# Performance work log

Hardware: AMD Instinct MI355X
Metric: run time of the kernel (lower is better)

## Reference

```python
import jax, jax.numpy as jnp
import numpy as np

N = 2_000_000
NODES = 16
FEAT = 19  # 9 (F) + 9 (cof F) + 1 (det F)


def setup_inputs() -> dict:
    key = jax.random.key(0)
    ks = jax.random.split(key, 9)
    # well-conditioned deformation gradients: F = I + 0.1*randn
    Fs = jnp.eye(3, dtype=jnp.float32) + 0.1 * jax.random.normal(ks[0], (N, 3, 3), dtype=jnp.float32)
    def glorot(k, shape):
        fan_in, fan_out = shape
        lim = np.sqrt(6.0 / (fan_in + fan_out)).astype(np.float32)
        return jax.random.uniform(k, shape, jnp.float32, -lim, lim)
    # layer 0: Dense(16, softplus); layers 1,2: Dense(16, softplus, non_neg kernel);
    # layer 3: Dense(1, linear, non_neg kernel). non_neg is a constraint applied
    # during training; we emulate by taking abs of the constrained kernels.
    W1 = glorot(ks[1], (FEAT, NODES)); b1 = jnp.zeros((NODES,), jnp.float32)
    W2 = jnp.abs(glorot(ks[2], (NODES, NODES))); b2 = jnp.zeros((NODES,), jnp.float32)
    W3 = jnp.abs(glorot(ks[3], (NODES, NODES))); b3 = jnp.zeros((NODES,), jnp.float32)
    W4 = jnp.abs(glorot(ks[4], (NODES, 1))); b4 = jnp.zeros((1,), jnp.float32)
    return {"Fs": Fs, "W1": W1, "b1": b1, "W2": W2, "b2": b2,
            "W3": W3, "b3": b3, "W4": W4, "b4": b4}


def _features(Fs):
    # det via closed-form 3x3 expansion (same value as tf.linalg.det)
    a, b, c = Fs[:, 0, 0], Fs[:, 0, 1], Fs[:, 0, 2]
    d, e, f = Fs[:, 1, 0], Fs[:, 1, 1], Fs[:, 1, 2]
    g, h, i = Fs[:, 2, 0], Fs[:, 2, 1], Fs[:, 2, 2]
    det = a * (e * i - f * h) - b * (d * i - f * g) + c * (d * h - e * g)
    # cof(F) = inv(F)^T * det  (original: transpose(inv(F)) @ diag(tile(det,3)))
    cof = jnp.swapaxes(jnp.linalg.inv(Fs), 1, 2) * det[:, None, None]
    # [N,19] = flat(F) ++ flat(cof) ++ det
    return jnp.concatenate([Fs.reshape(-1, 9), cof.reshape(-1, 9), det[:, None]], axis=1)


def reference(Fs, W1, b1, W2, b2, W3, b3, W4, b4):
    x = _features(Fs)
    x = jax.nn.softplus(x @ W1 + b1)
    x = jax.nn.softplus(x @ W2 + b2)
    x = jax.nn.softplus(x @ W3 + b3)
    return x @ W4 + b4  # [N,1]
```

## Files before the change

kernel.cpp:

```cpp
#include <hip/hip_runtime.h>
#include <hip/hip_fp16.h>
#include <math.h>

#define TPB 256
#define NODES 16
#define BLOCKS 2048

typedef float f32x4 __attribute__((ext_vector_type(4)));
typedef _Float16 half4 __attribute__((ext_vector_type(4)));
typedef _Float16 h2 __attribute__((ext_vector_type(2)));

#define LOG2E 1.44269504088896340736f
#define LN2   0.69314718055994530942f

__device__ __forceinline__ _Float16 hx2(_Float16 x) {
    __half h = __builtin_bit_cast(__half, x);
    __half r = hexp2(h);
    return __builtin_bit_cast(_Float16, r);
}

__device__ __forceinline__ unsigned int sp2_pos(float v0, float v1) {
    h2 h = __builtin_bit_cast(h2, __builtin_amdgcn_cvt_pkrtz(v0, v1));
    h2 e = { hx2((_Float16)(-h[0])), hx2((_Float16)(-h[1])) };
    const h2 c3 = {(_Float16)0.154358f,  (_Float16)0.154358f};
    const h2 c2 = {(_Float16)-0.571177f, (_Float16)-0.571177f};
    const h2 c1 = {(_Float16)1.416467f,  (_Float16)1.416467f};
    const h2 c0 = {(_Float16)0.000837f,  (_Float16)0.000837f};
    h2 p = __builtin_elementwise_fma(e,
             __builtin_elementwise_fma(e,
               __builtin_elementwise_fma(e, c3, c2), c1), c0);
    h2 r = h + p;
    return __builtin_bit_cast(unsigned int, r);
}
__device__ __forceinline__ unsigned int sp2_any(float v0, float v1) {
    h2 h = __builtin_bit_cast(h2, __builtin_amdgcn_cvt_pkrtz(v0, v1));
    const h2 z = {(_Float16)0.0f, (_Float16)0.0f};
    h2 m  = __builtin_elementwise_max(h, z);
    h2 nt = __builtin_elementwise_min(h, z - h);
    h2 e = { hx2(nt[0]), hx2(nt[1]) };
    const h2 c3 = {(_Float16)0.154358f,  (_Float16)0.154358f};
    const h2 c2 = {(_Float16)-0.571177f, (_Float16)-0.571177f};
    const h2 c1 = {(_Float16)1.416467f,  (_Float16)1.416467f};
    const h2 c0 = {(_Float16)0.000837f,  (_Float16)0.000837f};
    h2 p = __builtin_elementwise_fma(e,
             __builtin_elementwise_fma(e,
               __builtin_elementwise_fma(e, c3, c2), c1), c0);
    h2 r = m + p;
    return __builtin_bit_cast(unsigned int, r);
}
__device__ __forceinline__ unsigned int pk2(float a, float b) {
    return __builtin_bit_cast(unsigned int, __builtin_amdgcn_cvt_pkrtz(a, b));
}
__device__ __forceinline__ half4 h4(uint2 u) {
    return __builtin_bit_cast(half4, u);
}

__global__ __launch_bounds__(TPB, 4) void mlp_mfma_kernel(
    const float* __restrict__ Fs,
    const float* __restrict__ W1, const float* __restrict__ b1,
    const float* __restrict__ W2, const float* __restrict__ b2,
    const float* __restrict__ W3, const float* __restrict__ b3,
    const float* __restrict__ W4, const float* __restrict__ b4,
    float* __restrict__ out, int n, int iters)
{
    __shared__ uint2 lds[4][320];
    const int tid = threadIdx.x;
    const int l = tid & 63, w = tid >> 6;
    const int g = l >> 4, c = l & 15;

    half4 a1lo, a1hi, a2, a3, a4;
    f32x4 cb1, cb2, cb3, cb4;
    #pragma unroll
    for (int j = 0; j < 4; ++j) {
        a1lo[j] = (_Float16)(W1[(4*g+j)*NODES + c] * LOG2E);
        a1hi[j] = (_Float16)((g == 0 && j < 3) ? W1[(16+j)*NODES + c] * LOG2E : 0.0f);
        a2[j]   = (_Float16)W2[(4*g+j)*NODES + c];
        a3[j]   = (_Float16)W3[(4*g+j)*NODES + c];
        a4[j]   = (_Float16)(W4[4*g+j] * LN2);
    }
    const float b4s = b4[0];
    #pragma unroll
    for (int i = 0; i < 4; ++i) {
        cb1[i] = b1[4*g+i] * LOG2E;
        cb2[i] = b2[4*g+i] * LOG2E;
        cb3[i] = b3[4*g+i] * LOG2E;
        cb4[i] = b4s;
    }

    uint2* basep = &lds[w][0];
    const long long s0 = ((long long)blockIdx.x * 4 + w) * (64LL * iters);
    if (s0 >= n) return;

    float fr[9];
    {
        long long sE = s0 + l; if (sE > n - 1) sE = n - 1;
        const float* fp = Fs + sE * 9;
        #pragma unroll
        for (int q = 0; q < 9; ++q) fr[q] = fp[q];
    }

    for (int it = 0; it < iters; ++it) {
        long long ws = s0 + (long long)it * 64;
        if (ws >= n) break;

        float nf[9];
        const bool havenext = (it + 1 < iters) && (ws + 64 < n);
        if (havenext) {
            long long sE = ws + 64 + l; if (sE > n - 1) sE = n - 1;
            const float* fp = Fs + sE * 9;
            #pragma unroll
            for (int q = 0; q < 9; ++q) nf[q] = fp[q];
        }

        float a = fr[0], b = fr[1], cc = fr[2];
        float d = fr[3], e = fr[4], f5 = fr[5];
        float g7 = fr[6], h7 = fr[7], i8 = fr[8];

        float C00 = e * i8 - f5 * h7;
        float C01 = f5 * g7 - d * i8;
        float C02 = d * h7 - e * g7;
        float det = fmaf(a, C00, fmaf(b, C01, cc * C02));
        float C10 = cc * h7 - b * i8;
        float C11 = a * i8 - cc * g7;
        float C12 = b * g7 - a * h7;
        float C20 = b * f5 - cc * e;
        float C21 = cc * d - a * f5;
        float C22 = a * e - b * d;

        {
            uint2 v;
            v.x = pk2(a,   b);   v.y = pk2(cc,  d);   basep[l*5 + 0] = v;
            v.x = pk2(e,   f5);  v.y = pk2(g7,  h7);  basep[l*5 + 1] = v;
            v.x = pk2(i8,  C00); v.y = pk2(C01, C02); basep[l*5 + 2] = v;
            v.x = pk2(C10, C11); v.y = pk2(C12, C20); basep[l*5 + 3] = v;
            v.x = pk2(C21, C22); v.y = pk2(det, 0.0f); basep[l*5 + 4] = v;
        }
        asm volatile("s_waitcnt lgkmcnt(0)" ::: "memory");

        uint2 rlo0 = basep[(16*0 + c)*5 + g];
        uint2 rlo1 = basep[(16*1 + c)*5 + g];
        uint2 rlo2 = basep[(16*2 + c)*5 + g];
        uint2 rlo3 = basep[(16*3 + c)*5 + g];
        uint2 rhi0 = basep[(16*0 + c)*5 + 4];
        uint2 rhi1 = basep[(16*1 + c)*5 + 4];
        uint2 rhi2 = basep[(16*2 + c)*5 + 4];
        uint2 rhi3 = basep[(16*3 + c)*5 + 4];

        f32x4 t10 = __builtin_amdgcn_mfma_f32_16x16x16f16(a1lo, h4(rlo0), cb1, 0, 0, 0);
        f32x4 t11 = __builtin_amdgcn_mfma_f32_16x16x16f16(a1lo, h4(rlo1), cb1, 0, 0, 0);
        f32x4 t12 = __builtin_amdgcn_mfma_f32_16x16x16f16(a1lo, h4(rlo2), cb1, 0, 0, 0);
        f32x4 t13 = __builtin_amdgcn_mfma_f32_16x16x16f16(a1lo, h4(rlo3), cb1, 0, 0, 0);
        t10 = __builtin_amdgcn_mfma_f32_16x16x16f16(a1hi, h4(rhi0), t10, 0, 0, 0);
        t11 = __builtin_amdgcn_mfma_f32_16x16x16f16(a1hi, h4(rhi1), t11, 0, 0, 0);
        t12 = __builtin_amdgcn_mfma_f32_16x16x16f16(a1hi, h4(rhi2), t12, 0, 0, 0);
        t13 = __builtin_amdgcn_mfma_f32_16x16x16f16(a1hi, h4(rhi3), t13, 0, 0, 0);

        uint2 u0, u1, u2, u3;
        u0.x = sp2_any(t10[0], t10[1]); u0.y = sp2_any(t10[2], t10[3]);
        u1.x = sp2_any(t11[0], t11[1]); u1.y = sp2_any(t11[2], t11[3]);
        u2.x = sp2_any(t12[0], t12[1]); u2.y = sp2_any(t12[2], t12[3]);
        u3.x = sp2_any(t13[0], t13[1]); u3.y = sp2_any(t13[2], t13[3]);

        f32x4 d20 = __builtin_amdgcn_mfma_f32_16x16x16f16(a2, h4(u0), cb2, 0, 0, 0);
        f32x4 d21 = __builtin_amdgcn_mfma_f32_16x16x16f16(a2, h4(u1), cb2, 0, 0, 0);
        f32x4 d22 = __builtin_amdgcn_mfma_f32_16x16x16f16(a2, h4(u2), cb2, 0, 0, 0);
        f32x4 d23 = __builtin_amdgcn_mfma_f32_16x16x16f16(a2, h4(u3), cb2, 0, 0, 0);

        u0.x = sp2_pos(d20[0], d20[1]); u0.y = sp2_pos(d20[2], d20[3]);
        u1.x = sp2_pos(d21[0], d21[1]); u1.y = sp2_pos(d21[2], d21[3]);
        u2.x = sp2_pos(d22[0], d22[1]); u2.y = sp2_pos(d22[2], d22[3]);
        u3.x = sp2_pos(d23[0], d23[1]); u3.y = sp2_pos(d23[2], d23[3]);

        f32x4 d30 = __builtin_amdgcn_mfma_f32_16x16x16f16(a3, h4(u0), cb3, 0, 0, 0);
        f32x4 d31 = __builtin_amdgcn_mfma_f32_16x16x16f16(a3, h4(u1), cb3, 0, 0, 0);
        f32x4 d32 = __builtin_amdgcn_mfma_f32_16x16x16f16(a3, h4(u2), cb3, 0, 0, 0);
        f32x4 d33 = __builtin_amdgcn_mfma_f32_16x16x16f16(a3, h4(u3), cb3, 0, 0, 0);

        u0.x = sp2_pos(d30[0], d30[1]); u0.y = sp2_pos(d30[2], d30[3]);
        u1.x = sp2_pos(d31[0], d31[1]); u1.y = sp2_pos(d31[2], d31[3]);
        u2.x = sp2_pos(d32[0], d32[1]); u2.y = sp2_pos(d32[2], d32[3]);
        u3.x = sp2_pos(d33[0], d33[1]); u3.y = sp2_pos(d33[2], d33[3]);

        f32x4 d40 = __builtin_amdgcn_mfma_f32_16x16x16f16(a4, h4(u0), cb4, 0, 0, 0);
        f32x4 d41 = __builtin_amdgcn_mfma_f32_16x16x16f16(a4, h4(u1), cb4, 0, 0, 0);
        f32x4 d42 = __builtin_amdgcn_mfma_f32_16x16x16f16(a4, h4(u2), cb4, 0, 0, 0);
        f32x4 d43 = __builtin_amdgcn_mfma_f32_16x16x16f16(a4, h4(u3), cb4, 0, 0, 0);

        float yo = (g == 0) ? d40[0] : ((g == 1) ? d41[0] : ((g == 2) ? d42[0] : d43[0]));
        if (ws + l < n) out[ws + l] = yo;

        if (havenext) {
            #pragma unroll
            for (int q = 0; q < 9; ++q) fr[q] = nf[q];
        }
    }
}

extern "C" void kernel_launch(void* const* d_in, const int* in_sizes, int n_in,
                              void* d_out, int out_size, void* d_ws, size_t ws_size,
                              hipStream_t stream) {
    const float* Fs = (const float*)d_in[0];
    const float* W1 = (const float*)d_in[1];
    const float* b1 = (const float*)d_in[2];
    const float* W2 = (const float*)d_in[3];
    const float* b2 = (const float*)d_in[4];
    const float* W3 = (const float*)d_in[5];
    const float* b3 = (const float*)d_in[6];
    const float* W4 = (const float*)d_in[7];
    const float* b4 = (const float*)d_in[8];
    float* out = (float*)d_out;

    int n = in_sizes[0] / 9;
    int waves = (n + 63) / 64;
    int iters = (waves + BLOCKS * 4 - 1) / (BLOCKS * 4);
    mlp_mfma_kernel<<<BLOCKS, TPB, 0, stream>>>(Fs, W1, b1, W2, b2, W3, b3, W4, b4,
                                                out, n, iters);
}
```

Before: 30.21 us.

## Process two 64-sample tiles per wave iteration with interleaved MFMA chains

Each wave now handles 128 samples per loop iteration using two LDS buffers and two independent MFMA/softplus chains, interleaved A/B so the matrix unit has independent work to hide dependency latency. The prefetch of the next tile's inputs moves to after the feature stores, and iteration count is halved. This raises register pressure (two sets of 9 prefetched floats and accumulators) under launch_bounds(256,4), which may cause spills or reduce occupancy.

After: 31.00 us. 2.6% more time.

```diff
diff --git a/kernel.cpp b/kernel.cpp
--- a/kernel.cpp
+++ b/kernel.cpp
@@ -63,7 +63,7 @@
     const float* __restrict__ W4, const float* __restrict__ b4,
     float* __restrict__ out, int n, int iters)
 {
-    __shared__ uint2 lds[4][320];
+    __shared__ uint2 lds[4][2][320];
     const int tid = threadIdx.x;
     const int l = tid & 63, w = tid >> 6;
     const int g = l >> 4, c = l & 15;
@@ -87,113 +87,157 @@
         cb4[i] = b4s;
     }
 
-    uint2* basep = &lds[w][0];
-    const long long s0 = ((long long)blockIdx.x * 4 + w) * (64LL * iters);
+    uint2* basepA = &lds[w][0][0];
+    uint2* basepB = &lds[w][1][0];
+    const long long s0 = ((long long)blockIdx.x * 4 + w) * (128LL * iters);
     if (s0 >= n) return;
 
-    float fr[9];
-    {
-        long long sE = s0 + l; if (sE > n - 1) sE = n - 1;
-        const float* fp = Fs + sE * 9;
-        #pragma unroll
-        for (int q = 0; q < 9; ++q) fr[q] = fp[q];
+    float frA[9], frB[9];
+
+    #define LOADF(R, S)                                                          \
+        do {                                                                     \
+            long long sE = (S) + l; if (sE > n - 1) sE = n - 1;                  \
+            const float* fp = Fs + sE * 9;                                       \
+            _Pragma("unroll")                                                    \
+            for (int q = 0; q < 9; ++q) (R)[q] = fp[q];                          \
+        } while (0)
+
+    #define FEATW(R, B)                                                          \
+        do {                                                                     \
+            float a = (R)[0], b = (R)[1], cc = (R)[2];                           \
+            float d = (R)[3], e = (R)[4], f5 = (R)[5];                           \
+            float g7 = (R)[6], h7 = (R)[7], i8 = (R)[8];                         \
+            float C00 = e * i8 - f5 * h7;                                        \
+            float C01 = f5 * g7 - d * i8;                                        \
+            float C02 = d * h7 - e * g7;                                         \
+            float det = fmaf(a, C00, fmaf(b, C01, cc * C02));                    \
+            float C10 = cc * h7 - b * i8;                                        \
+            float C11 = a * i8 - cc * g7;                                        \
+            float C12 = b * g7 - a * h7;                                         \
+            float C20 = b * f5 - cc * e;                                         \
+            float C21 = cc * d - a * f5;                                         \
+            float C22 = a * e - b * d;                                           \
+            uint2 v;                                                             \
+            v.x = pk2(a,   b);   v.y = pk2(cc,  d);    (B)[l*5 + 0] = v;         \
+            v.x = pk2(e,   f5);  v.y = pk2(g7,  h7);   (B)[l*5 + 1] = v;         \
+            v.x = pk2(i8,  C00); v.y = pk2(C01, C02);  (B)[l*5 + 2] = v;         \
+            v.x = pk2(C10, C11); v.y = pk2(C12, C20);  (B)[l*5 + 3] = v;         \
+            v.x = pk2(C21, C22); v.y = pk2(det, 0.0f); (B)[l*5 + 4] = v;         \
+        } while (0)
+
+    LOADF(frA, s0);
+    LOADF(frB, s0 + 64);
+
+    for (int it = 0; it < iters; ++it) {
+        long long ws = s0 + (long long)it * 128;
+        if (ws >= n) break;
+
+        FEATW(frA, basepA);
+        FEATW(frB, basepB);
+        asm volatile("s_waitcnt lgkmcnt(0)" ::: "memory");
+
+        const bool havenext = (it + 1 < iters) && (ws + 128 < n);
+        if (havenext) {
+            LOADF(frA, ws + 128);
+            LOADF(frB, ws + 192);
+        }
+
+        uint2 Alo0 = basepA[(16*0 + c)*5 + g];
+        uint2 Alo1 = basepA[(16*1 + c)*5 + g];
+        uint2 Alo2 = basepA[(16*2 + c)*5 + g];
+        uint2 Alo3 = basepA[(16*3 + c)*5 + g];
+        uint2 Ahi0 = basepA[(16*0 + c)*5 + 4];
+        uint2 Ahi1 = basepA[(16*1 + c)*5 + 4];
+        uint2 Ahi2 = basepA[(16*2 + c)*5 + 4];
+        uint2 Ahi3 = basepA[(16*3 + c)*5 + 4];
+        uint2 Blo0 = basepB[(16*0 + c)*5 + g];
+        uint2 Blo1 = basepB[(16*1 + c)*5 + g];
+        uint2 Blo2 = basepB[(16*2 + c)*5 + g];
+        uint2 Blo3 = basepB[(16*3 + c)*5 + g];
+        uint2 Bhi0 = basepB[(16*0 + c)*5 + 4];
+        uint2 Bhi1 = basepB[(16*1 + c)*5 + 4];
+        uint2 Bhi2 = basepB[(16*2 + c)*5 + 4];
+        uint2 Bhi3 = basepB[(16*3 + c)*5 + 4];
+
+        f32x4 tA0 = __builtin_amdgcn_mfma_f32_16x16x16f16(a1lo, h4(Alo0), cb1, 0, 0, 0);
+        f32x4 tB0 = __builtin_amdgcn_mfma_f32_16x16x16f16(a1lo, h4(Blo0), cb1, 0, 0, 0);
+        f32x4 tA1 = __builtin_amdgcn_mfma_f32_16x16x16f16(a1lo, h4(Alo1), cb1, 0, 0, 0);
+        f32x4 tB1 = __builtin_amdgcn_mfma_f32_16x16x16f16(a1lo, h4(Blo1), cb1, 0, 0, 0);
+        f32x4 tA2 = __builtin_amdgcn_mfma_f32_16x16x16f16(a1lo, h4(Alo2), cb1, 0, 0, 0);
+        f32x4 tB2 = __builtin_amdgcn_mfma_f32_16x16x16f16(a1lo, h4(Blo2), cb1, 0, 0, 0);
+        f32x4 tA3 = __builtin_amdgcn_mfma_f32_16x16x16f16(a1lo, h4(Alo3), cb1, 0, 0, 0);
+        f32x4 tB3 = __builtin_amdgcn_mfma_f32_16x16x16f16(a1lo, h4(Blo3), cb1, 0, 0, 0);
+        tA0 = __builtin_amdgcn_mfma_f32_16x16x16f16(a1hi, h4(Ahi0), tA0, 0, 0, 0);
+        tB0 = __builtin_amdgcn_mfma_f32_16x16x16f16(a1hi, h4(Bhi0), tB0, 0, 0, 0);
+        tA1 = __builtin_amdgcn_mfma_f32_16x16x16f16(a1hi, h4(Ahi1), tA1, 0, 0, 0);
+        tB1 = __builtin_amdgcn_mfma_f32_16x16x16f16(a1hi, h4(Bhi1), tB1, 0, 0, 0);
+        tA2 = __builtin_amdgcn_mfma_f32_16x16x16f16(a1hi, h4(Ahi2), tA2, 0, 0, 0);
+        tB2 = __builtin_amdgcn_mfma_f32_16x16x16f16(a1hi, h4(Bhi2), tB2, 0, 0, 0);
+        tA3 = __builtin_amdgcn_mfma_f32_16x16x16f16(a1hi, h4(Ahi3), tA3, 0, 0, 0);
+        tB3 = __builtin_amdgcn_mfma_f32_16x16x16f16(a1hi, h4(Bhi3), tB3, 0, 0, 0);
+
+        uint2 uA0, uA1, uA2, uA3, uB0, uB1, uB2, uB3;
+        uA0.x = sp2_any(tA0[0], tA0[1]); uA0.y = sp2_any(tA0[2], tA0[3]);
+        uB0.x = sp2_any(tB0[0], tB0[1]); uB0.y = sp2_any(tB0[2], tB0[3]);
+        uA1.x = sp2_any(tA1[0], tA1[1]); uA1.y = sp2_any(tA1[2], tA1[3]);
+        uB1.x = sp2_any(tB1[0], tB1[1]); uB1.y = sp2_any(tB1[2], tB1[3]);
+        uA2.x = sp2_any(tA2[0], tA2[1]); uA2.y = sp2_any(tA2[2], tA2[3]);
+        uB2.x = sp2_any(tB2[0], tB2[1]); uB2.y = sp2_any(tB2[2], tB2[3]);
+        uA3.x = sp2_any(tA3[0], tA3[1]); uA3.y = sp2_any(tA3[2], tA3[3]);
+        uB3.x = sp2_any(tB3[0], tB3[1]); uB3.y = sp2_any(tB3[2], tB3[3]);
+
+        f32x4 dA0 = __builtin_amdgcn_mfma_f32_16x16x16f16(a2, h4(uA0), cb2, 0, 0, 0);
+        f32x4 dB0 = __builtin_amdgcn_mfma_f32_16x16x16f16(a2, h4(uB0), cb2, 0, 0, 0);
+        f32x4 dA1 = __builtin_amdgcn_mfma_f32_16x16x16f16(a2, h4(uA1), cb2, 0, 0, 0);
+        f32x4 dB1 = __builtin_amdgcn_mfma_f32_16x16x16f16(a2, h4(uB1), cb2, 0, 0, 0);
+        f32x4 dA2 = __builtin_amdgcn_mfma_f32_16x16x16f16(a2, h4(uA2), cb2, 0, 0, 0);
+        f32x4 dB2 = __builtin_amdgcn_mfma_f32_16x16x16f16(a2, h4(uB2), cb2, 0, 0, 0);
+        f32x4 dA3 = __builtin_amdgcn_mfma_f32_16x16x16f16(a2, h4(uA3), cb2, 0, 0, 0);
+        f32x4 dB3 = __builtin_amdgcn_mfma_f32_16x16x16f16(a2, h4(uB3), cb2, 0, 0, 0);
+
+        uA0.x = sp2_pos(dA0[0], dA0[1]); uA0.y = sp2_pos(dA0[2], dA0[3]);
+        uB0.x = sp2_pos(dB0[0], dB0[1]); uB0.y = sp2_pos(dB0[2], dB0[3]);
+        uA1.x = sp2_pos(dA1[0], dA1[1]); uA1.y = sp2_pos(dA1[2], dA1[3]);
+        uB1.x = sp2_pos(dB1[0], dB1[1]); uB1.y = sp2_pos(dB1[2], dB1[3]);
+        uA2.x = sp2_pos(dA2[0], dA2[1]); uA2.y = sp2_pos(dA2[2], dA2[3]);
+        uB2.x = sp2_pos(dB2[0], dB2[1]); uB2.y = sp2_pos(dB2[2], dB2[3]);
+        uA3.x = sp2_pos(dA3[0], dA3[1]); uA3.y = sp2_pos(dA3[2], dA3[3]);
+        uB3.x = sp2_pos(dB3[0], dB3[1]); uB3.y = sp2_pos(dB3[2], dB3[3]);
+
+        dA0 = __builtin_amdgcn_mfma_f32_16x16x16f16(a3, h4(uA0), cb3, 0, 0, 0);
+        dB0 = __builtin_amdgcn_mfma_f32_16x16x16f16(a3, h4(uB0), cb3, 0, 0, 0);
+        dA1 = __builtin_amdgcn_mfma_f32_16x16x16f16(a3, h4(uA1), cb3, 0, 0, 0);
+        dB1 = __builtin_amdgcn_mfma_f32_16x16x16f16(a3, h4(uB1), cb3, 0, 0, 0);
+        dA2 = __builtin_amdgcn_mfma_f32_16x16x16f16(a3, h4(uA2), cb3, 0, 0, 0);
+        dB2 = __builtin_amdgcn_mfma_f32_16x16x16f16(a3, h4(uB2), cb3, 0, 0, 0);
+        dA3 = __builtin_amdgcn_mfma_f32_16x16x16f16(a3, h4(uA3), cb3, 0, 0, 0);
+        dB3 = __builtin_amdgcn_mfma_f32_16x16x16f16(a3, h4(uB3), cb3, 0, 0, 0);
+
+        uA0.x = sp2_pos(dA0[0], dA0[1]); uA0.y = sp2_pos(dA0[2], dA0[3]);
+        uB0.x = sp2_pos(dB0[0], dB0[1]); uB0.y = sp2_pos(dB0[2], dB0[3]);
+        uA1.x = sp2_pos(dA1[0], dA1[1]); uA1.y = sp2_pos(dA1[2], dA1[3]);
+        uB1.x = sp2_pos(dB1[0], dB1[1]); uB1.y = sp2_pos(dB1[2], dB1[3]);
+        uA2.x = sp2_pos(dA2[0], dA2[1]); uA2.y = sp2_pos(dA2[2], dA2[3]);
+        uB2.x = sp2_pos(dB2[0], dB2[1]); uB2.y = sp2_pos(dB2[2], dB2[3]);
+        uA3.x = sp2_pos(dA3[0], dA3[1]); uA3.y = sp2_pos(dA3[2], dA3[3]);
+        uB3.x = sp2_pos(dB3[0], dB3[1]); uB3.y = sp2_pos(dB3[2], dB3[3]);
+
+        f32x4 eA0 = __builtin_amdgcn_mfma_f32_16x16x16f16(a4, h4(uA0), cb4, 0, 0, 0);
+        f32x4 eB0 = __builtin_amdgcn_mfma_f32_16x16x16f16(a4, h4(uB0), cb4, 0, 0, 0);
+        f32x4 eA1 = __builtin_amdgcn_mfma_f32_16x16x16f16(a4, h4(uA1), cb4, 0, 0, 0);
+        f32x4 eB1 = __builtin_amdgcn_mfma_f32_16x16x16f16(a4, h4(uB1), cb4, 0, 0, 0);
+        f32x4 eA2 = __builtin_amdgcn_mfma_f32_16x16x16f16(a4, h4(uA2), cb4, 0, 0, 0);
+        f32x4 eB2 = __builtin_amdgcn_mfma_f32_16x16x16f16(a4, h4(uB2), cb4, 0, 0, 0);
+        f32x4 eA3 = __builtin_amdgcn_mfma_f32_16x16x16f16(a4, h4(uA3), cb4, 0, 0, 0);
+        f32x4 eB3 = __builtin_amdgcn_mfma_f32_16x16x16f16(a4, h4(uB3), cb4, 0, 0, 0);
+
+        float yA = (g == 0) ? eA0[0] : ((g == 1) ? eA1[0] : ((g == 2) ? eA2[0] : eA3[0]));
+        float yB = (g == 0) ? eB0[0] : ((g == 1) ? eB1[0] : ((g == 2) ? eB2[0] : eB3[0]));
+        if (ws + l < n)      out[ws + l] = yA;
+        if (ws + 64 + l < n) out[ws + 64 + l] = yB;
     }
-
-    for (int it = 0; it < iters; ++it) {
-        long long ws = s0 + (long long)it * 64;
-        if (ws >= n) break;
-
-        float nf[9];
-        const bool havenext = (it + 1 < iters) && (ws + 64 < n);
-        if (havenext) {
-            long long sE = ws + 64 + l; if (sE > n - 1) sE = n - 1;
-            const float* fp = Fs + sE * 9;
-            #pragma unroll
-            for (int q = 0; q < 9; ++q) nf[q] = fp[q];
-        }
-
-        float a = fr[0], b = fr[1], cc = fr[2];
-        float d = fr[3], e = fr[4], f5 = fr[5];
-        float g7 = fr[6], h7 = fr[7], i8 = fr[8];
-
-        float C00 = e * i8 - f5 * h7;
-        float C01 = f5 * g7 - d * i8;
-        float C02 = d * h7 - e * g7;
-        float det = fmaf(a, C00, fmaf(b, C01, cc * C02));
-        float C10 = cc * h7 - b * i8;
-        float C11 = a * i8 - cc * g7;
-        float C12 = b * g7 - a * h7;
-        float C20 = b * f5 - cc * e;
-        float C21 = cc * d - a * f5;
-        float C22 = a * e - b * d;
-
-        {
-            uint2 v;
-            v.x = pk2(a,   b);   v.y = pk2(cc,  d);   basep[l*5 + 0] = v;
-            v.x = pk2(e,   f5);  v.y = pk2(g7,  h7);  basep[l*5 + 1] = v;
-            v.x = pk2(i8,  C00); v.y = pk2(C01, C02); basep[l*5 + 2] = v;
-            v.x = pk2(C10, C11); v.y = pk2(C12, C20); basep[l*5 + 3] = v;
-            v.x = pk2(C21, C22); v.y = pk2(det, 0.0f); basep[l*5 + 4] = v;
-        }
-        asm volatile("s_waitcnt lgkmcnt(0)" ::: "memory");
-
-        uint2 rlo0 = basep[(16*0 + c)*5 + g];
-        uint2 rlo1 = basep[(16*1 + c)*5 + g];
-        uint2 rlo2 = basep[(16*2 + c)*5 + g];
-        uint2 rlo3 = basep[(16*3 + c)*5 + g];
-        uint2 rhi0 = basep[(16*0 + c)*5 + 4];
-        uint2 rhi1 = basep[(16*1 + c)*5 + 4];
-        uint2 rhi2 = basep[(16*2 + c)*5 + 4];
-        uint2 rhi3 = basep[(16*3 + c)*5 + 4];
-
-        f32x4 t10 = __builtin_amdgcn_mfma_f32_16x16x16f16(a1lo, h4(rlo0), cb1, 0, 0, 0);
-        f32x4 t11 = __builtin_amdgcn_mfma_f32_16x16x16f16(a1lo, h4(rlo1), cb1, 0, 0, 0);
-        f32x4 t12 = __builtin_amdgcn_mfma_f32_16x16x16f16(a1lo, h4(rlo2), cb1, 0, 0, 0);
-        f32x4 t13 = __builtin_amdgcn_mfma_f32_16x16x16f16(a1lo, h4(rlo3), cb1, 0, 0, 0);
-        t10 = __builtin_amdgcn_mfma_f32_16x16x16f16(a1hi, h4(rhi0), t10, 0, 0, 0);
-        t11 = __builtin_amdgcn_mfma_f32_16x16x16f16(a1hi, h4(rhi1), t11, 0, 0, 0);
-        t12 = __builtin_amdgcn_mfma_f32_16x16x16f16(a1hi, h4(rhi2), t12, 0, 0, 0);
-        t13 = __builtin_amdgcn_mfma_f32_16x16x16f16(a1hi, h4(rhi3), t13, 0, 0, 0);
-
-        uint2 u0, u1, u2, u3;
-        u0.x = sp2_any(t10[0], t10[1]); u0.y = sp2_any(t10[2], t10[3]);
-        u1.x = sp2_any(t11[0], t11[1]); u1.y = sp2_any(t11[2], t11[3]);
-        u2.x = sp2_any(t12[0], t12[1]); u2.y = sp2_any(t12[2], t12[3]);
-        u3.x = sp2_any(t13[0], t13[1]); u3.y = sp2_any(t13[2], t13[3]);
-
-        f32x4 d20 = __builtin_amdgcn_mfma_f32_16x16x16f16(a2, h4(u0), cb2, 0, 0, 0);
-        f32x4 d21 = __builtin_amdgcn_mfma_f32_16x16x16f16(a2, h4(u1), cb2, 0, 0, 0);
-        f32x4 d22 = __builtin_amdgcn_mfma_f32_16x16x16f16(a2, h4(u2), cb2, 0, 0, 0);
-        f32x4 d23 = __builtin_amdgcn_mfma_f32_16x16x16f16(a2, h4(u3), cb2, 0, 0, 0);
-
-        u0.x = sp2_pos(d20[0], d20[1]); u0.y = sp2_pos(d20[2], d20[3]);
-        u1.x = sp2_pos(d21[0], d21[1]); u1.y = sp2_pos(d21[2], d21[3]);
-        u2.x = sp2_pos(d22[0], d22[1]); u2.y = sp2_pos(d22[2], d22[3]);
-        u3.x = sp2_pos(d23[0], d23[1]); u3.y = sp2_pos(d23[2], d23[3]);
-
-        f32x4 d30 = __builtin_amdgcn_mfma_f32_16x16x16f16(a3, h4(u0), cb3, 0, 0, 0);
-        f32x4 d31 = __builtin_amdgcn_mfma_f32_16x16x16f16(a3, h4(u1), cb3, 0, 0, 0);
-        f32x4 d32 = __builtin_amdgcn_mfma_f32_16x16x16f16(a3, h4(u2), cb3, 0, 0, 0);
-        f32x4 d33 = __builtin_amdgcn_mfma_f32_16x16x16f16(a3, h4(u3), cb3, 0, 0, 0);
-
-        u0.x = sp2_pos(d30[0], d30[1]); u0.y = sp2_pos(d30[2], d30[3]);
-        u1.x = sp2_pos(d31[0], d31[1]); u1.y = sp2_pos(d31[2], d31[3]);
-        u2.x = sp2_pos(d32[0], d32[1]); u2.y = sp2_pos(d32[2], d32[3]);
-        u3.x = sp2_pos(d33[0], d33[1]); u3.y = sp2_pos(d33[2], d33[3]);
-
-        f32x4 d40 = __builtin_amdgcn_mfma_f32_16x16x16f16(a4, h4(u0), cb4, 0, 0, 0);
-        f32x4 d41 = __builtin_amdgcn_mfma_f32_16x16x16f16(a4, h4(u1), cb4, 0, 0, 0);
-        f32x4 d42 = __builtin_amdgcn_mfma_f32_16x16x16f16(a4, h4(u2), cb4, 0, 0, 0);
-        f32x4 d43 = __builtin_amdgcn_mfma_f32_16x16x16f16(a4, h4(u3), cb4, 0, 0, 0);
-
-        float yo = (g == 0) ? d40[0] : ((g == 1) ? d41[0] : ((g == 2) ? d42[0] : d43[0]));
-        if (ws + l < n) out[ws + l] = yo;
-
-        if (havenext) {
-            #pragma unroll
-            for (int q = 0; q < 9; ++q) fr[q] = nf[q];
-        }
-    }
+    #undef LOADF
+    #undef FEATW
 }
 
 extern "C" void kernel_launch(void* const* d_in, const int* in_sizes, int n_in,
@@ -211,8 +255,9 @@
     float* out = (float*)d_out;
 
     int n = in_sizes[0] / 9;
-    int waves = (n + 63) / 64;
-    int iters = (waves + BLOCKS * 4 - 1) / (BLOCKS * 4);
+    long long per_wave = 128;
+    long long waves = (long long)BLOCKS * 4;
+    int iters = (int)((n + waves * per_wave - 1) / (waves * per_wave));
     mlp_mfma_kernel<<<BLOCKS, TPB, 0, stream>>>(Fs, W1, b1, W2, b2, W3, b3, W4, b4,
                                                 out, n, iters);
 }
```
